# Kernel tuning notes

Measured on AMD Instinct MI355X. Metric: run time of the kernel, lower is better.

## Reference

```python
import jax, jax.numpy as jnp
import numpy as np

N_HEADS = 4


def _fq_sym(x, qmax=127.0):
    # symmetric per-tensor dynamic int8 fake-quant with straight-through estimator
    scale = jnp.maximum(jnp.max(jnp.abs(x)) / qmax, 1e-8)
    q = jnp.clip(jnp.round(x / scale), -qmax, qmax) * scale
    return x + jax.lax.stop_gradient(q - x)


def _fq_unsigned(x, qmax=255.0):
    # unsigned 8-bit fake-quant (for softmax probabilities in [0,1])
    scale = jnp.maximum(jnp.max(x) / qmax, 1e-8)
    q = jnp.clip(jnp.round(x / scale), 0.0, qmax) * scale
    return x + jax.lax.stop_gradient(q - x)


def setup_inputs() -> dict:
    key = jax.random.key(0)
    kq, kk, kv = jax.random.split(key, 3)
    shape = (16, 256, 32, 32)  # [B, n_heads*head_dim, H, W]
    return {
        "q": jax.random.normal(kq, shape, dtype=jnp.float32),
        "k": jax.random.normal(kk, shape, dtype=jnp.float32),
        "v": jax.random.normal(kv, shape, dtype=jnp.float32),
    }


def reference(q, k, v):
    b, c, h, w = q.shape
    d = c // N_HEADS
    s = h * w

    def split_heads(x):
        # b (n d) h w -> b n (h w) d
        return jnp.swapaxes(x.reshape(b, N_HEADS, d, s), -1, -2)

    qh, kh, vh = split_heads(q), split_heads(k), split_heads(v)  # [b,n,s,d]
    scale = d ** (-0.5)

    # QuanMMHead: fake-quantize both operands, then matmul, scaled by 1/sqrt(d)
    attn = jnp.einsum("bnsd,bntd->bnst", _fq_sym(qh), _fq_sym(kh)) * scale
    # QuanSoftmax: softmax then fake-quantize probabilities
    attn = _fq_unsigned(jax.nn.softmax(attn, axis=-1))
    # QuanMMHead for attn @ V
    out = jnp.einsum("bnst,bntd->bnsd", _fq_sym(attn), _fq_sym(vh))  # [b,n,s,d]

    # b n s d -> b (n d) h w
    out = jnp.swapaxes(out, -1, -2).reshape(b, c, h, w)
    return out
```

## Files before the change

kernel.cpp:

```cpp
#include <hip/hip_runtime.h>
#include <math.h>

#define NBN 64
#define DD  64
#define SS  1024

typedef int i32x4_ __attribute__((ext_vector_type(4)));

#if defined(__has_builtin)
#  if __has_builtin(__builtin_amdgcn_exp2f)
#    define FEXP2(x) __builtin_amdgcn_exp2f(x)
#  endif
#endif
#ifndef FEXP2
#  define FEXP2(x) exp2f(x)
#endif

#if defined(__has_builtin)
#  if __has_builtin(__builtin_amdgcn_cvt_pk_u8_f32)
#    define PK_U8(f, r, old) __builtin_amdgcn_cvt_pk_u8_f32((f), (r), (old))
#  endif
#endif
#ifndef PK_U8
#  define PK_U8(f, r, old) (((old) & ~(0xff << (8*(r)))) | (((int)(f) & 0xff) << (8*(r))))
#endif

__device__ __forceinline__ i32x4_ mfma_i8(i32x4_ a, i32x4_ b, i32x4_ c) {
    return __builtin_amdgcn_mfma_i32_16x16x64_i8(a, b, c, 0, 0, 0);
}

__device__ __forceinline__ int quant_sym(float x, float sc) {
    float r = fminf(fmaxf(rintf(x / sc), -127.0f), 127.0f);
    return (int)r;
}

__device__ __forceinline__ float wave_max256(const float* part, int lane) {
    float4 t = ((const float4*)part)[lane];
    float m = fmaxf(fmaxf(t.x, t.y), fmaxf(t.z, t.w));
    #pragma unroll
    for (int mk = 1; mk <= 32; mk <<= 1) m = fmaxf(m, __shfl_xor(m, mk, 64));
    return m;
}

__device__ __forceinline__ float wave_min2048(const float* part, int lane) {
    float4 t = ((const float4*)part)[lane];
    float m = fminf(fminf(t.x, t.y), fminf(t.z, t.w));
    #pragma unroll
    for (int i = 1; i < 8; ++i) {
        float4 u = ((const float4*)part)[lane + i * 64];
        m = fminf(m, fminf(fminf(u.x, u.y), fminf(u.z, u.w)));
    }
    #pragma unroll
    for (int mk = 1; mk <= 32; mk <<= 1) m = fminf(m, __shfl_xor(m, mk, 64));
    return m;
}

__global__ void k_absmax(const float* __restrict__ q, const float* __restrict__ k,
                         const float* __restrict__ v, float* __restrict__ amax_part) {
    const float* src = (blockIdx.y == 0) ? q : (blockIdx.y == 1) ? k : v;
    const int n = NBN * DD * SS;
    float m = 0.0f;
    for (int i = (blockIdx.x * 256 + threadIdx.x) * 4; i < n; i += gridDim.x * 256 * 4) {
        float4 x = *(const float4*)(src + i);
        m = fmaxf(m, fmaxf(fmaxf(fabsf(x.x), fabsf(x.y)), fmaxf(fabsf(x.z), fabsf(x.w))));
    }
    __shared__ float red[256];
    red[threadIdx.x] = m;
    __syncthreads();
    for (int off = 128; off > 0; off >>= 1) {
        if (threadIdx.x < off) red[threadIdx.x] = fmaxf(red[threadIdx.x], red[threadIdx.x + off]);
        __syncthreads();
    }
    if (threadIdx.x == 0) amax_part[blockIdx.y * 256 + blockIdx.x] = red[0];
}

__global__ void k_quant_qkv(const float* __restrict__ q, const float* __restrict__ k,
                            const float* __restrict__ v, const float* __restrict__ amax_part,
                            int* __restrict__ Qp, int* __restrict__ Kp, int* __restrict__ Vq) {
    __shared__ float TlA[64][69];
    __shared__ __align__(16) int TlB[64][20];
    const int which = blockIdx.z;
    const int bn = blockIdx.y;
    const int tid = threadIdx.x;
    const float sc = fmaxf(wave_max256(amax_part + which * 256, tid & 63) / 127.0f, 1e-8f);
    if (which < 2) {
        const float* tsrc = (which ? k : q) + (size_t)bn * DD * SS;
        int* dst = which ? Kp : Qp;
        const int s_base = blockIdx.x * 64;
        #pragma unroll
        for (int kk = 0; kk < 4; ++kk) {
            int idx = tid + kk * 256;
            int d = idx >> 4, s4 = idx & 15;
            float4 x = *(const float4*)(tsrc + (size_t)d * SS + s_base + s4 * 4);
            TlA[d][s4*4+0] = x.x; TlA[d][s4*4+1] = x.y;
            TlA[d][s4*4+2] = x.z; TlA[d][s4*4+3] = x.w;
        }
        __syncthreads();
        const int u = tid & 3, s_loc = tid >> 2;
        int pw[4];
        #pragma unroll
        for (int jj = 0; jj < 4; ++jj) {
            int p = 0;
            #pragma unroll
            for (int r = 0; r < 4; ++r) {
                int iq = quant_sym(TlA[16*u + 4*jj + r][s_loc], sc);
                p |= (iq & 0xff) << (8 * r);
            }
            pw[jj] = p;
        }
        *(int4*)(dst + ((size_t)bn * SS + s_base + s_loc) * 16 + u * 4)
            = make_int4(pw[0], pw[1], pw[2], pw[3]);
    } else {
        const int tb = blockIdx.x;
        {
            const int d = tid >> 2, tqq = tid & 3;
            #pragma unroll
            for (int i = 0; i < 4; ++i) {
                const int tq = tqq * 4 + i;
                float4 x = *(const float4*)(v + (size_t)(bn * 64 + d) * SS + tb * 64 + tq * 4);
                TlB[d][tq] = (quant_sym(x.x, sc) & 0xff)
                          | ((quant_sym(x.y, sc) & 0xff) << 8)
                          | ((quant_sym(x.z, sc) & 0xff) << 16)
                          | ((quant_sym(x.w, sc) & 0xff) << 24);
            }
        }
        __syncthreads();
        {
            const int dt = tid >> 6, gg = (tid >> 4) & 3;
            const int d = dt * 16 + (tid & 15);
            int4 w = make_int4(TlB[d][gg*4+0], TlB[d][gg*4+1], TlB[d][gg*4+2], TlB[d][gg*4+3]);
            *(int4*)(Vq + (size_t)(bn * 16 + tb) * 1024 + tid * 4) = w;
        }
    }
}

__global__ __launch_bounds__(512) void k_phase_a(const int* __restrict__ Qp,
    const int* __restrict__ Kp, const float* __restrict__ amax_part,
    float* __restrict__ m2_arr, float* __restrict__ l_arr, float* __restrict__ minl_part)
{
    __shared__ float Mf[8][32];
    __shared__ float Lf[8][32];
    const int x = blockIdx.x;
    const int bn = ((x & 7) << 3) | ((x >> 3) & 7);
    const int s0 = blockIdx.y * 32;
    const int tid = threadIdx.x;
    const int wv = tid >> 6, lane = tid & 63;
    const int g = lane >> 4, c = lane & 15;
    const float aq = wave_max256(amax_part, lane);
    const float ak = wave_max256(amax_part + 256, lane);
    const float sq = fmaxf(aq / 127.0f, 1e-8f);
    const float sk = fmaxf(ak / 127.0f, 1e-8f);
    const float cqk2 = (sq * sk * 0.125f) * 1.4426950408889634f;
    const i32x4_ qf0 = *(const i32x4_*)(Qp + ((size_t)bn * SS + s0 + c) * 16 + g * 4);
    const i32x4_ qf1 = *(const i32x4_*)(Qp + ((size_t)bn * SS + s0 + 16 + c) * 16 + g * 4);
    const i32x4_ zero = {0, 0, 0, 0};
    const int* kb = Kp + ((size_t)bn * SS + wv * 128 + c) * 16 + g * 4;

    i32x4_ kfr[8];
    #pragma unroll
    for (int j = 0; j < 8; ++j) kfr[j] = *(const i32x4_*)(kb + j * 256);
    __builtin_amdgcn_sched_barrier(0);
    i32x4_ dq0[8], dq1[8];
    #pragma unroll
    for (int j = 0; j < 8; ++j) {
        dq0[j] = mfma_i8(kfr[j], qf0, zero);
        dq1[j] = mfma_i8(kfr[j], qf1, zero);
    }

    int im0 = -2147483647, im1 = -2147483647;
    #pragma unroll
    for (int j = 0; j < 8; ++j) {
        im0 = max(im0, max(max(dq0[j][0], dq0[j][1]), max(dq0[j][2], dq0[j][3])));
        im1 = max(im1, max(max(dq1[j][0], dq1[j][1]), max(dq1[j][2], dq1[j][3])));
    }
    im0 = max(im0, __shfl_xor(im0, 16, 64));
    im0 = max(im0, __shfl_xor(im0, 32, 64));
    im1 = max(im1, __shfl_xor(im1, 16, 64));
    im1 = max(im1, __shfl_xor(im1, 32, 64));
    const float m0 = (float)im0 * cqk2;
    const float m1 = (float)im1 * cqk2;
    float la0 = 0.0f, lb0 = 0.0f, lc0 = 0.0f, ld0 = 0.0f;
    float la1 = 0.0f, lb1 = 0.0f, lc1 = 0.0f, ld1 = 0.0f;
    #pragma unroll
    for (int j = 0; j < 8; ++j) {
        la0 += FEXP2(fmaf((float)dq0[j][0], cqk2, -m0));
        lb0 += FEXP2(fmaf((float)dq0[j][1], cqk2, -m0));
        lc0 += FEXP2(fmaf((float)dq0[j][2], cqk2, -m0));
        ld0 += FEXP2(fmaf((float)dq0[j][3], cqk2, -m0));
        la1 += FEXP2(fmaf((float)dq1[j][0], cqk2, -m1));
        lb1 += FEXP2(fmaf((float)dq1[j][1], cqk2, -m1));
        lc1 += FEXP2(fmaf((float)dq1[j][2], cqk2, -m1));
        ld1 += FEXP2(fmaf((float)dq1[j][3], cqk2, -m1));
    }
    float l0 = (la0 + lb0) + (lc0 + ld0);
    float l1 = (la1 + lb1) + (lc1 + ld1);
    l0 += __shfl_xor(l0, 16, 64);
    l0 += __shfl_xor(l0, 32, 64);
    l1 += __shfl_xor(l1, 16, 64);
    l1 += __shfl_xor(l1, 32, 64);
    if (g == 0) {
        Mf[wv][c] = m0;      Lf[wv][c] = l0;
        Mf[wv][16 + c] = m1; Lf[wv][16 + c] = l1;
    }
    __syncthreads();
    if (tid < 32) {
        const int cc = tid;
        float m = Mf[0][cc];
        #pragma unroll
        for (int w = 1; w < 8; ++w) m = fmaxf(m, Mf[w][cc]);
        float l = 0.0f;
        #pragma unroll
        for (int w = 0; w < 8; ++w) l += Lf[w][cc] * FEXP2(Mf[w][cc] - m);
        m2_arr[bn * SS + s0 + cc] = m;
        l_arr[bn * SS + s0 + cc] = l;
        float lm = l;
        #pragma unroll
        for (int mk = 1; mk <= 16; mk <<= 1) lm = fminf(lm, __shfl_xor(lm, mk, 64));
        if (cc == 0) minl_part[blockIdx.y * 64 + blockIdx.x] = lm;
    }
}

__global__ __launch_bounds__(512, 8) void k_phase_b(const int* __restrict__ Qp,
    const int* __restrict__ Kp, const int* __restrict__ Vq,
    const float* __restrict__ amax_part, const float* __restrict__ minl_part,
    const float* __restrict__ m2_arr, const float* __restrict__ l_arr,
    float* __restrict__ out)
{
    __shared__ __align__(16) int POOL[6912];
    const int f = blockIdx.x + (blockIdx.y << 4);
    const int bn = ((f & 7) << 3) | ((f >> 3) & 7);
    const int sblk = (f >> 6) * 64;
    const int tid = threadIdx.x;
    const int wv = tid >> 6, lane = tid & 63;
    const int g = lane >> 4, c = lane & 15;
    const int sgrp = wv & 3, th = wv >> 2;
    const int s0 = sblk + sgrp * 16;
    const float sq = fmaxf(wave_max256(amax_part, lane) / 127.0f, 1e-8f);
    const float sk = fmaxf(wave_max256(amax_part + 256, lane) / 127.0f, 1e-8f);
    const float sv = fmaxf(wave_max256(amax_part + 512, lane) / 127.0f, 1e-8f);
    const float minl = wave_min2048(minl_part, lane);
    const float cqk2 = (sq * sk * 0.125f) * 1.4426950408889634f;
    const float maxP     = 1.0f / minl;
    const float scale_p  = fmaxf(maxP / 255.0f, 1e-8f);
    const float scale_p2 = fmaxf((255.0f * scale_p) / 127.0f, 1e-8f);
    const float cpv = scale_p2 * sv;
    const float m2 = m2_arr[bn * SS + s0 + c];
    const float l  = l_arr [bn * SS + s0 + c];
    const float bexp = log2f((1.0f / scale_p) / l) - m2;
    const i32x4_ qf = *(const i32x4_*)(Qp + ((size_t)bn * SS + s0 + c) * 16 + g * 4);
    const i32x4_ zero = {0, 0, 0, 0};
    int* Kst = POOL + th * 1024;
    int* Vst = POOL + 2048 + th * 1024;
    int* myP = POOL + 4096 + wv * 320;
    const int woff = c * 20 + g * 4;
    const int tb0 = th * 8;
    const int soff = sgrp * 256 + lane * 4;
    const int* kg = Kp + (size_t)bn * SS * 16 + soff;
    const int* vg = Vq + (size_t)bn * 16384 + soff;

    i32x4_ acc[4] = {zero, zero, zero, zero};

    {
        i32x4_ gk = *(const i32x4_*)(kg + tb0 * 1024);
        i32x4_ gv = *(const i32x4_*)(vg + tb0 * 1024);
        *(i32x4_*)&Kst[soff] = gk;
        *(i32x4_*)&Vst[soff] = gv;
    }
    __syncthreads();

    #pragma unroll
    for (int i = 0; i < 8; ++i) {
        i32x4_ gk, gv;
        if (i < 7) {
            gk = *(const i32x4_*)(kg + (tb0 + i + 1) * 1024);
            gv = *(const i32x4_*)(vg + (tb0 + i + 1) * 1024);
        }
        __builtin_amdgcn_sched_barrier(0);
        int W[4];
        #pragma unroll
        for (int j = 0; j < 4; ++j) {
            i32x4_ kf = *(const i32x4_*)&Kst[j * 256 + c * 16 + g * 4];
            i32x4_ dq = mfma_i8(kf, qf, zero);
            int w = 0;
            #pragma unroll
            for (int r = 0; r < 4; ++r) {
                float xx = FEXP2(fmaf((float)dq[r], cqk2, bexp));
                w = PK_U8(rintf(xx), r, w);
            }
            W[j] = (w >> 1) & 0x7f7f7f7f;
        }
        i32x4_ wv4 = {W[0], W[1], W[2], W[3]};
        *(i32x4_*)(myP + woff) = wv4;
        i32x4_ pa;
        pa[0] = myP[c * 20 + 0 + g];
        pa[1] = myP[c * 20 + 4 + g];
        pa[2] = myP[c * 20 + 8 + g];
        pa[3] = myP[c * 20 + 12 + g];
        #pragma unroll
        for (int dt = 0; dt < 4; ++dt) {
            i32x4_ vf = *(const i32x4_*)&Vst[dt * 256 + g * 64 + c * 4];
            acc[dt] = mfma_i8(pa, vf, acc[dt]);
        }
        __syncthreads();
        if (i < 7) {
            *(i32x4_*)&Kst[soff] = gk;
            *(i32x4_*)&Vst[soff] = gv;
            __syncthreads();
        }
    }

    int* sbuf = POOL;
    if (th == 0) {
        #pragma unroll
        for (int dt = 0; dt < 4; ++dt)
            #pragma unroll
            for (int r = 0; r < 4; ++r)
                sbuf[(dt * 16 + c) * 67 + sgrp * 16 + 4 * g + r] = acc[dt][r];
    }
    __syncthreads();
    if (th == 1) {
        #pragma unroll
        for (int dt = 0; dt < 4; ++dt)
            #pragma unroll
            for (int r = 0; r < 4; ++r) {
                const int slot = (dt * 16 + c) * 67 + sgrp * 16 + 4 * g + r;
                ((float*)sbuf)[slot] = (float)(sbuf[slot] + acc[dt][r]) * cpv;
            }
    }
    __syncthreads();
    #pragma unroll
    for (int u = 0; u < 2; ++u) {
        const int chunk = tid + u * 512;
        const int d = chunk >> 4, sq4 = chunk & 15;
        const float* fb = (const float*)sbuf + d * 67 + sq4 * 4;
        float4 val = make_float4(fb[0], fb[1], fb[2], fb[3]);
        *(float4*)(out + (size_t)bn * 65536 + (size_t)d * 1024 + sblk + sq4 * 4) = val;
    }
}

extern "C" void kernel_launch(void* const* d_in, const int* in_sizes, int n_in,
                              void* d_out, int out_size, void* d_ws, size_t ws_size,
                              hipStream_t stream) {
    const float* q = (const float*)d_in[0];
    const float* k = (const float*)d_in[1];
    const float* v = (const float*)d_in[2];
    float* out = (float*)d_out;
    char* ws = (char*)d_ws;

    float* amax_part = (float*)ws;
    float* minl_part = (float*)(ws + 4096);
    int* Qp      = (int*)(ws + 16384);
    int* Kp      = (int*)(ws + 16384 + (size_t)(1 << 22));
    int* Vq      = (int*)(ws + 16384 + (size_t)(2 << 22));
    float* m2    = (float*)(ws + 16384 + (size_t)(3 << 22));
    float* l_a   = (float*)(ws + 16384 + (size_t)(3 << 22) + (1 << 18));

    k_absmax<<<dim3(256, 3), 256, 0, stream>>>(q, k, v, amax_part);
    k_quant_qkv<<<dim3(16, NBN, 3), 256, 0, stream>>>(q, k, v, amax_part, Qp, Kp, Vq);
    k_phase_a<<<dim3(64, 32), 512, 0, stream>>>(Qp, Kp, amax_part, m2, l_a, minl_part);
    k_phase_b<<<dim3(16, NBN), 512, 0, stream>>>(Qp, Kp, Vq, amax_part, minl_part, m2, l_a, out);
}
```

Measured before the change: 66.80 us.

## Fuse four kernel launches into one persistent kernel with grid barriers

Replaces the four separate launches (absmax, quantize, softmax stats, PV) with a single persistent kernel whose grid is sized from occupancy times CU count. Phases are separated by software grid barriers built on atomics, and the previous per-block work is distributed by looping over work units. The goal is to remove launch gaps and per-kernel tail effects. In exchange it adds host-side occupancy and device-property queries on every call, a memset, and the risk of deadlock if not all blocks are co-resident. It also changes the ordering of phase-A blocks, which were previously swizzled for locality.

```diff
diff --git a/kernel.cpp b/kernel.cpp
--- a/kernel.cpp
+++ b/kernel.cpp
@@ -53,6 +53,308 @@
     #pragma unroll
     for (int mk = 1; mk <= 32; mk <<= 1) m = fminf(m, __shfl_xor(m, mk, 64));
     return m;
+}
+
+__device__ __forceinline__ void gbar(unsigned* bar, unsigned nb) {
+    __syncthreads();
+    if (threadIdx.x == 0) {
+        __threadfence();
+        unsigned g = __hip_atomic_load(bar + 1, __ATOMIC_RELAXED, __HIP_MEMORY_SCOPE_AGENT);
+        unsigned old = __hip_atomic_fetch_add(bar, 1u, __ATOMIC_ACQ_REL, __HIP_MEMORY_SCOPE_AGENT);
+        if (old == nb - 1u) {
+            __hip_atomic_store(bar, 0u, __ATOMIC_RELAXED, __HIP_MEMORY_SCOPE_AGENT);
+            __hip_atomic_fetch_add(bar + 1, 1u, __ATOMIC_RELEASE, __HIP_MEMORY_SCOPE_AGENT);
+        } else {
+            while (__hip_atomic_load(bar + 1, __ATOMIC_ACQUIRE, __HIP_MEMORY_SCOPE_AGENT) == g)
+                __builtin_amdgcn_s_sleep(2);
+        }
+        __threadfence();
+    }
+    __syncthreads();
+}
+
+__global__ __launch_bounds__(512) void k_mega(
+    const float* __restrict__ q, const float* __restrict__ k, const float* __restrict__ v,
+    float* __restrict__ amax_part, float* __restrict__ minl_part,
+    int* __restrict__ Qp, int* __restrict__ Kp, int* __restrict__ Vq,
+    float* __restrict__ m2_arr, float* __restrict__ l_arr,
+    float* __restrict__ out, unsigned* __restrict__ bar)
+{
+    __shared__ __align__(16) int POOL[6912];
+    const unsigned nb = gridDim.x;
+    const int bid = blockIdx.x, tid = threadIdx.x;
+    const int lane = tid & 63;
+    const i32x4_ zero = {0, 0, 0, 0};
+
+    for (int u = bid; u < 768; u += nb) {
+        const int t = u >> 8, slice = u & 255;
+        const float* src = (t == 0) ? q : (t == 1) ? k : v;
+        const float4* s4 = (const float4*)src + slice * 4096;
+        float m = 0.0f;
+        #pragma unroll
+        for (int j = 0; j < 8; ++j) {
+            float4 x = s4[j * 512 + tid];
+            m = fmaxf(m, fmaxf(fmaxf(fabsf(x.x), fabsf(x.y)), fmaxf(fabsf(x.z), fabsf(x.w))));
+        }
+        float* red = (float*)POOL;
+        red[tid] = m;
+        __syncthreads();
+        for (int off = 256; off > 0; off >>= 1) {
+            if (tid < off) red[tid] = fmaxf(red[tid], red[tid + off]);
+            __syncthreads();
+        }
+        if (tid == 0) amax_part[t * 256 + slice] = red[0];
+        __syncthreads();
+    }
+    gbar(bar, nb);
+
+    for (int u = bid; u < 3072; u += nb) {
+        if (u < 2048) {
+            const int which = u >> 10, bn = (u >> 4) & 63, chunk = u & 15;
+            const float sc = fmaxf(wave_max256(amax_part + which * 256, lane) / 127.0f, 1e-8f);
+            const float* tsrc = (which ? k : q) + (size_t)bn * DD * SS;
+            int* dst = which ? Kp : Qp;
+            const int s_base = chunk * 64;
+            float* TlA = (float*)POOL;
+            #pragma unroll
+            for (int it = 0; it < 2; ++it) {
+                const int idx = tid + it * 512;
+                const int d = idx >> 4, s4i = idx & 15;
+                float4 x = *(const float4*)(tsrc + (size_t)d * SS + s_base + s4i * 4);
+                TlA[d * 69 + s4i * 4 + 0] = x.x; TlA[d * 69 + s4i * 4 + 1] = x.y;
+                TlA[d * 69 + s4i * 4 + 2] = x.z; TlA[d * 69 + s4i * 4 + 3] = x.w;
+            }
+            __syncthreads();
+            if (tid < 256) {
+                const int uu = tid & 3, s_loc = tid >> 2;
+                int pw[4];
+                #pragma unroll
+                for (int jj = 0; jj < 4; ++jj) {
+                    int p = 0;
+                    #pragma unroll
+                    for (int r = 0; r < 4; ++r) {
+                        int iq = quant_sym(TlA[(16 * uu + 4 * jj + r) * 69 + s_loc], sc);
+                        p |= (iq & 0xff) << (8 * r);
+                    }
+                    pw[jj] = p;
+                }
+                *(int4*)(dst + ((size_t)bn * SS + s_base + s_loc) * 16 + uu * 4)
+                    = make_int4(pw[0], pw[1], pw[2], pw[3]);
+            }
+            __syncthreads();
+        } else {
+            const int vv = u - 2048, bn = vv >> 4, tb = vv & 15;
+            const float sc = fmaxf(wave_max256(amax_part + 512, lane) / 127.0f, 1e-8f);
+            int* TlB = POOL;
+            #pragma unroll
+            for (int it = 0; it < 2; ++it) {
+                const int idx = tid + it * 512;
+                const int d = idx >> 4, tq = idx & 15;
+                float4 x = *(const float4*)(v + (size_t)(bn * 64 + d) * SS + tb * 64 + tq * 4);
+                TlB[d * 20 + tq] = (quant_sym(x.x, sc) & 0xff)
+                                | ((quant_sym(x.y, sc) & 0xff) << 8)
+                                | ((quant_sym(x.z, sc) & 0xff) << 16)
+                                | ((quant_sym(x.w, sc) & 0xff) << 24);
+            }
+            __syncthreads();
+            if (tid < 256) {
+                const int dt = tid >> 6, gg = (tid >> 4) & 3;
+                const int d = dt * 16 + (tid & 15);
+                int4 w = make_int4(TlB[d * 20 + gg * 4 + 0], TlB[d * 20 + gg * 4 + 1],
+                                   TlB[d * 20 + gg * 4 + 2], TlB[d * 20 + gg * 4 + 3]);
+                *(int4*)(Vq + (size_t)(bn * 16 + tb) * 1024 + tid * 4) = w;
+            }
+            __syncthreads();
+        }
+    }
+    gbar(bar + 2, nb);
+
+    {
+        const float sq = fmaxf(wave_max256(amax_part, lane) / 127.0f, 1e-8f);
+        const float sk = fmaxf(wave_max256(amax_part + 256, lane) / 127.0f, 1e-8f);
+        const float cqk2 = (sq * sk * 0.125f) * 1.4426950408889634f;
+        const int wv = tid >> 6;
+        const int g = lane >> 4, c = lane & 15;
+        float* Mf = (float*)POOL;
+        float* Lf = (float*)POOL + 256;
+        for (int u = bid; u < 2048; u += nb) {
+            const int bn = u >> 5, s0 = (u & 31) * 32;
+            const i32x4_ qf0 = *(const i32x4_*)(Qp + ((size_t)bn * SS + s0 + c) * 16 + g * 4);
+            const i32x4_ qf1 = *(const i32x4_*)(Qp + ((size_t)bn * SS + s0 + 16 + c) * 16 + g * 4);
+            const int* kb = Kp + ((size_t)bn * SS + wv * 128 + c) * 16 + g * 4;
+            i32x4_ kfr[8];
+            #pragma unroll
+            for (int j = 0; j < 8; ++j) kfr[j] = *(const i32x4_*)(kb + j * 256);
+            __builtin_amdgcn_sched_barrier(0);
+            i32x4_ dq0[8], dq1[8];
+            #pragma unroll
+            for (int j = 0; j < 8; ++j) {
+                dq0[j] = mfma_i8(kfr[j], qf0, zero);
+                dq1[j] = mfma_i8(kfr[j], qf1, zero);
+            }
+            int im0 = -2147483647, im1 = -2147483647;
+            #pragma unroll
+            for (int j = 0; j < 8; ++j) {
+                im0 = max(im0, max(max(dq0[j][0], dq0[j][1]), max(dq0[j][2], dq0[j][3])));
+                im1 = max(im1, max(max(dq1[j][0], dq1[j][1]), max(dq1[j][2], dq1[j][3])));
+            }
+            im0 = max(im0, __shfl_xor(im0, 16, 64));
+            im0 = max(im0, __shfl_xor(im0, 32, 64));
+            im1 = max(im1, __shfl_xor(im1, 16, 64));
+            im1 = max(im1, __shfl_xor(im1, 32, 64));
+            const float m0 = (float)im0 * cqk2;
+            const float m1 = (float)im1 * cqk2;
+            float la0 = 0.f, lb0 = 0.f, lc0 = 0.f, ld0 = 0.f;
+            float la1 = 0.f, lb1 = 0.f, lc1 = 0.f, ld1 = 0.f;
+            #pragma unroll
+            for (int j = 0; j < 8; ++j) {
+                la0 += FEXP2(fmaf((float)dq0[j][0], cqk2, -m0));
+                lb0 += FEXP2(fmaf((float)dq0[j][1], cqk2, -m0));
+                lc0 += FEXP2(fmaf((float)dq0[j][2], cqk2, -m0));
+                ld0 += FEXP2(fmaf((float)dq0[j][3], cqk2, -m0));
+                la1 += FEXP2(fmaf((float)dq1[j][0], cqk2, -m1));
+                lb1 += FEXP2(fmaf((float)dq1[j][1], cqk2, -m1));
+                lc1 += FEXP2(fmaf((float)dq1[j][2], cqk2, -m1));
+                ld1 += FEXP2(fmaf((float)dq1[j][3], cqk2, -m1));
+            }
+            float l0 = (la0 + lb0) + (lc0 + ld0);
+            float l1 = (la1 + lb1) + (lc1 + ld1);
+            l0 += __shfl_xor(l0, 16, 64);
+            l0 += __shfl_xor(l0, 32, 64);
+            l1 += __shfl_xor(l1, 16, 64);
+            l1 += __shfl_xor(l1, 32, 64);
+            if (g == 0) {
+                Mf[wv * 32 + c] = m0;      Lf[wv * 32 + c] = l0;
+                Mf[wv * 32 + 16 + c] = m1; Lf[wv * 32 + 16 + c] = l1;
+            }
+            __syncthreads();
+            if (tid < 32) {
+                const int cc = tid;
+                float m = Mf[cc];
+                #pragma unroll
+                for (int w = 1; w < 8; ++w) m = fmaxf(m, Mf[w * 32 + cc]);
+                float l = 0.0f;
+                #pragma unroll
+                for (int w = 0; w < 8; ++w) l += Lf[w * 32 + cc] * FEXP2(Mf[w * 32 + cc] - m);
+                m2_arr[bn * SS + s0 + cc] = m;
+                l_arr[bn * SS + s0 + cc] = l;
+                float lm = l;
+                #pragma unroll
+                for (int mk = 1; mk <= 16; mk <<= 1) lm = fminf(lm, __shfl_xor(lm, mk, 64));
+                if (cc == 0) minl_part[u] = lm;
+            }
+            __syncthreads();
+        }
+    }
+    gbar(bar + 4, nb);
+
+    {
+        const float sq = fmaxf(wave_max256(amax_part, lane) / 127.0f, 1e-8f);
+        const float sk = fmaxf(wave_max256(amax_part + 256, lane) / 127.0f, 1e-8f);
+        const float sv = fmaxf(wave_max256(amax_part + 512, lane) / 127.0f, 1e-8f);
+        const float minl = wave_min2048(minl_part, lane);
+        const float cqk2 = (sq * sk * 0.125f) * 1.4426950408889634f;
+        const float maxP     = 1.0f / minl;
+        const float scale_p  = fmaxf(maxP / 255.0f, 1e-8f);
+        const float scale_p2 = fmaxf((255.0f * scale_p) / 127.0f, 1e-8f);
+        const float cpv = scale_p2 * sv;
+        const float rsl = 1.0f / scale_p;
+        const int wv = tid >> 6;
+        const int g = lane >> 4, c = lane & 15;
+        const int sgrp = wv & 3, th = wv >> 2;
+        const int tb0 = th * 8;
+        const int soff = sgrp * 256 + lane * 4;
+        int* Kst = POOL + th * 1024;
+        int* Vst = POOL + 2048 + th * 1024;
+        int* myP = POOL + 4096 + wv * 320;
+        const int woff = c * 20 + g * 4;
+        for (int u = bid; u < 1024; u += nb) {
+            const int bn = u >> 4, sblk = (u & 15) * 64;
+            const int s0 = sblk + sgrp * 16;
+            const float m2 = m2_arr[bn * SS + s0 + c];
+            const float l  = l_arr [bn * SS + s0 + c];
+            const float bexp = log2f(rsl / l) - m2;
+            const i32x4_ qf = *(const i32x4_*)(Qp + ((size_t)bn * SS + s0 + c) * 16 + g * 4);
+            const int* kg = Kp + (size_t)bn * SS * 16 + soff;
+            const int* vg = Vq + (size_t)bn * 16384 + soff;
+            i32x4_ acc[4] = {zero, zero, zero, zero};
+            {
+                i32x4_ gk = *(const i32x4_*)(kg + tb0 * 1024);
+                i32x4_ gv = *(const i32x4_*)(vg + tb0 * 1024);
+                *(i32x4_*)&Kst[soff] = gk;
+                *(i32x4_*)&Vst[soff] = gv;
+            }
+            __syncthreads();
+            #pragma unroll
+            for (int i = 0; i < 8; ++i) {
+                i32x4_ gk, gv;
+                if (i < 7) {
+                    gk = *(const i32x4_*)(kg + (tb0 + i + 1) * 1024);
+                    gv = *(const i32x4_*)(vg + (tb0 + i + 1) * 1024);
+                }
+                __builtin_amdgcn_sched_barrier(0);
+                int W[4];
+                #pragma unroll
+                for (int j = 0; j < 4; ++j) {
+                    i32x4_ kf = *(const i32x4_*)&Kst[j * 256 + c * 16 + g * 4];
+                    i32x4_ dq = mfma_i8(kf, qf, zero);
+                    int w = 0;
+                    #pragma unroll
+                    for (int r = 0; r < 4; ++r) {
+                        float xx = FEXP2(fmaf((float)dq[r], cqk2, bexp));
+                        w = PK_U8(rintf(xx), r, w);
+                    }
+                    W[j] = (w >> 1) & 0x7f7f7f7f;
+                }
+                i32x4_ wv4 = {W[0], W[1], W[2], W[3]};
+                *(i32x4_*)(myP + woff) = wv4;
+                i32x4_ pa;
+                pa[0] = myP[c * 20 + 0 + g];
+                pa[1] = myP[c * 20 + 4 + g];
+                pa[2] = myP[c * 20 + 8 + g];
+                pa[3] = myP[c * 20 + 12 + g];
+                #pragma unroll
+                for (int dt = 0; dt < 4; ++dt) {
+                    i32x4_ vf = *(const i32x4_*)&Vst[dt * 256 + g * 64 + c * 4];
+                    acc[dt] = mfma_i8(pa, vf, acc[dt]);
+                }
+                __syncthreads();
+                if (i < 7) {
+                    *(i32x4_*)&Kst[soff] = gk;
+                    *(i32x4_*)&Vst[soff] = gv;
+                    __syncthreads();
+                }
+            }
+            int* sbuf = POOL;
+            if (th == 0) {
+                #pragma unroll
+                for (int dt = 0; dt < 4; ++dt)
+                    #pragma unroll
+                    for (int r = 0; r < 4; ++r)
+                        sbuf[(dt * 16 + c) * 67 + sgrp * 16 + 4 * g + r] = acc[dt][r];
+            }
+            __syncthreads();
+            if (th == 1) {
+                #pragma unroll
+                for (int dt = 0; dt < 4; ++dt)
+                    #pragma unroll
+                    for (int r = 0; r < 4; ++r) {
+                        const int slot = (dt * 16 + c) * 67 + sgrp * 16 + 4 * g + r;
+                        ((float*)sbuf)[slot] = (float)(sbuf[slot] + acc[dt][r]) * cpv;
+                    }
+            }
+            __syncthreads();
+            #pragma unroll
+            for (int uu = 0; uu < 2; ++uu) {
+                const int chunk = tid + uu * 512;
+                const int d = chunk >> 4, s4i = chunk & 15;
+                const float* fb = (const float*)sbuf + d * 67 + s4i * 4;
+                float4 val = make_float4(fb[0], fb[1], fb[2], fb[3]);
+                *(float4*)(out + (size_t)bn * 65536 + (size_t)d * 1024 + sblk + s4i * 4) = val;
+            }
+            __syncthreads();
+        }
+    }
 }
 
 __global__ void k_absmax(const float* __restrict__ q, const float* __restrict__ k,
@@ -146,16 +448,13 @@
     const int tid = threadIdx.x;
     const int wv = tid >> 6, lane = tid & 63;
     const int g = lane >> 4, c = lane & 15;
-    const float aq = wave_max256(amax_part, lane);
-    const float ak = wave_max256(amax_part + 256, lane);
-    const float sq = fmaxf(aq / 127.0f, 1e-8f);
-    const float sk = fmaxf(ak / 127.0f, 1e-8f);
+    const float sq = fmaxf(wave_max256(amax_part, lane) / 127.0f, 1e-8f);
+    const float sk = fmaxf(wave_max256(amax_part + 256, lane) / 127.0f, 1e-8f);
     const float cqk2 = (sq * sk * 0.125f) * 1.4426950408889634f;
     const i32x4_ qf0 = *(const i32x4_*)(Qp + ((size_t)bn * SS + s0 + c) * 16 + g * 4);
     const i32x4_ qf1 = *(const i32x4_*)(Qp + ((size_t)bn * SS + s0 + 16 + c) * 16 + g * 4);
     const i32x4_ zero = {0, 0, 0, 0};
     const int* kb = Kp + ((size_t)bn * SS + wv * 128 + c) * 16 + g * 4;
-
     i32x4_ kfr[8];
     #pragma unroll
     for (int j = 0; j < 8; ++j) kfr[j] = *(const i32x4_*)(kb + j * 256);
@@ -166,7 +465,6 @@
         dq0[j] = mfma_i8(kfr[j], qf0, zero);
         dq1[j] = mfma_i8(kfr[j], qf1, zero);
     }
-
     int im0 = -2147483647, im1 = -2147483647;
     #pragma unroll
     for (int j = 0; j < 8; ++j) {
@@ -179,8 +477,8 @@
     im1 = max(im1, __shfl_xor(im1, 32, 64));
     const float m0 = (float)im0 * cqk2;
     const float m1 = (float)im1 * cqk2;
-    float la0 = 0.0f, lb0 = 0.0f, lc0 = 0.0f, ld0 = 0.0f;
-    float la1 = 0.0f, lb1 = 0.0f, lc1 = 0.0f, ld1 = 0.0f;
+    float la0 = 0.f, lb0 = 0.f, lc0 = 0.f, ld0 = 0.f;
+    float la1 = 0.f, lb1 = 0.f, lc1 = 0.f, ld1 = 0.f;
     #pragma unroll
     for (int j = 0; j < 8; ++j) {
         la0 += FEXP2(fmaf((float)dq0[j][0], cqk2, -m0));
@@ -257,9 +555,7 @@
     const int soff = sgrp * 256 + lane * 4;
     const int* kg = Kp + (size_t)bn * SS * 16 + soff;
     const int* vg = Vq + (size_t)bn * 16384 + soff;
-
     i32x4_ acc[4] = {zero, zero, zero, zero};
-
     {
         i32x4_ gk = *(const i32x4_*)(kg + tb0 * 1024);
         i32x4_ gv = *(const i32x4_*)(vg + tb0 * 1024);
@@ -267,7 +563,6 @@
         *(i32x4_*)&Vst[soff] = gv;
     }
     __syncthreads();
-
     #pragma unroll
     for (int i = 0; i < 8; ++i) {
         i32x4_ gk, gv;
@@ -308,7 +603,6 @@
             __syncthreads();
         }
     }
-
     int* sbuf = POOL;
     if (th == 0) {
         #pragma unroll
@@ -331,10 +625,10 @@
     #pragma unroll
     for (int u = 0; u < 2; ++u) {
         const int chunk = tid + u * 512;
-        const int d = chunk >> 4, sq4 = chunk & 15;
-        const float* fb = (const float*)sbuf + d * 67 + sq4 * 4;
+        const int d = chunk >> 4, s4i = chunk & 15;
+        const float* fb = (const float*)sbuf + d * 67 + s4i * 4;
         float4 val = make_float4(fb[0], fb[1], fb[2], fb[3]);
-        *(float4*)(out + (size_t)bn * 65536 + (size_t)d * 1024 + sblk + sq4 * 4) = val;
+        *(float4*)(out + (size_t)bn * 65536 + (size_t)d * 1024 + sblk + s4i * 4) = val;
     }
 }
 
@@ -347,16 +641,32 @@
     float* out = (float*)d_out;
     char* ws = (char*)d_ws;
 
-    float* amax_part = (float*)ws;
-    float* minl_part = (float*)(ws + 4096);
+    unsigned* bar    = (unsigned*)ws;
+    float* amax_part = (float*)(ws + 1024);
+    float* minl_part = (float*)(ws + 8192);
     int* Qp      = (int*)(ws + 16384);
     int* Kp      = (int*)(ws + 16384 + (size_t)(1 << 22));
     int* Vq      = (int*)(ws + 16384 + (size_t)(2 << 22));
     float* m2    = (float*)(ws + 16384 + (size_t)(3 << 22));
     float* l_a   = (float*)(ws + 16384 + (size_t)(3 << 22) + (1 << 18));
 
-    k_absmax<<<dim3(256, 3), 256, 0, stream>>>(q, k, v, amax_part);
-    k_quant_qkv<<<dim3(16, NBN, 3), 256, 0, stream>>>(q, k, v, amax_part, Qp, Kp, Vq);
-    k_phase_a<<<dim3(64, 32), 512, 0, stream>>>(Qp, Kp, amax_part, m2, l_a, minl_part);
-    k_phase_b<<<dim3(16, NBN), 512, 0, stream>>>(Qp, Kp, Vq, amax_part, minl_part, m2, l_a, out);
-}
+    int bpc = 0;
+    hipError_t oe = hipOccupancyMaxActiveBlocksPerMultiprocessor(&bpc, k_mega, 512, 0);
+    int ncu = 256;
+    hipDeviceProp_t prop;
+    int dev = 0;
+    if (hipGetDevice(&dev) == hipSuccess && hipGetDeviceProperties(&prop, dev) == hipSuccess)
+        ncu = prop.multiProcessorCount;
+
+    if (oe == hipSuccess && bpc >= 1) {
+        int G = bpc * ncu;
+        if (G > 1024) G = 1024;
+        hipMemsetAsync(bar, 0, 64, stream);
+        k_mega<<<G, 512, 0, stream>>>(q, k, v, amax_part, minl_part, Qp, Kp, Vq, m2, l_a, out, bar);
+    } else {
+        k_absmax<<<dim3(256, 3), 256, 0, stream>>>(q, k, v, amax_part);
+        k_quant_qkv<<<dim3(16, NBN, 3), 256, 0, stream>>>(q, k, v, amax_part, Qp, Kp, Vq);
+        k_phase_a<<<dim3(64, 32), 512, 0, stream>>>(Qp, Kp, amax_part, m2, l_a, minl_part);
+        k_phase_b<<<dim3(16, NBN), 512, 0, stream>>>(Qp, Kp, Vq, amax_part, minl_part, m2, l_a, out);
+    }
+}
```

After: 198.6 us. 2.97x slower.
